# Kernel tuning notes

Measured on AMD Instinct MI355X. Metric: run time of the kernel, lower is better.

Reference implementation:

```python
import jax, jax.numpy as jnp
import numpy as np

SR = 8                      # search_range
MO = 2 * SR + 1             # max_offset = 17
NC = MO * MO                # 289 cost-volume channels


def _l2_normalize(x, eps=1e-12):
    # torch F.normalize(p=2, dim=1): x / max(||x||_2, eps)
    n = jnp.sqrt(jnp.sum(x * x, axis=1, keepdims=True))
    return x / jnp.maximum(n, eps)


def _conv2d(x, w, b, pad, groups=1):
    out = jax.lax.conv_general_dilated(
        x, w, window_strides=(1, 1), padding=[(pad, pad), (pad, pad)],
        feature_group_count=groups,
        dimension_numbers=('NCHW', 'OIHW', 'NCHW'))
    return out + b[None, :, None, None]


def _cost_volume(x1, x2, sr, norm_both=False):
    x1 = _l2_normalize(x1)
    if norm_both:
        x2 = _l2_normalize(x2)
    bs, c, h, w = x1.shape
    padded = jnp.pad(x2, ((0, 0), (0, 0), (sr, sr), (sr, sr)))
    mo = 2 * sr + 1
    # offsets in (j outer, i inner) order, matching the original double loop
    jj, ii = jnp.meshgrid(jnp.arange(mo), jnp.arange(mo), indexing='ij')
    offs = jnp.stack([jj.reshape(-1), ii.reshape(-1)], axis=-1)  # [mo^2, 2]

    def step(carry, off):
        sl = jax.lax.dynamic_slice(padded, (0, 0, off[0], off[1]), (bs, c, h, w))
        return carry, jnp.mean(x1 * sl, axis=1)  # [bs, h, w]

    _, cv = jax.lax.scan(step, None, offs)       # [mo^2, bs, h, w]
    cv = jnp.transpose(cv, (1, 0, 2, 3))          # [bs, mo^2, h, w]
    return jax.nn.leaky_relu(cv, 0.1)


def setup_inputs() -> dict:
    key = jax.random.key(0)
    ks = jax.random.split(key, 8)
    bs, c, h, w = 4, 256, 64, 64
    scale = 0.05
    return {
        'f1': jax.random.normal(ks[0], (bs, c, h, w), jnp.float32),
        'f2': jax.random.normal(ks[1], (bs, c, h, w), jnp.float32),
        'att_w': jax.random.normal(ks[2], (NC, 1, 7, 7), jnp.float32) * scale,
        'att_b': jax.random.normal(ks[3], (NC,), jnp.float32) * scale,
        'agg1_w': jax.random.normal(ks[4], (NC // 2, NC, 3, 3), jnp.float32) * scale,
        'agg1_b': jax.random.normal(ks[5], (NC // 2,), jnp.float32) * scale,
        'agg2_w': jax.random.normal(ks[6], (49, NC // 2, 3, 3), jnp.float32) * scale,
        'agg2_b': jax.random.normal(ks[7], (49,), jnp.float32) * scale,
    }


def reference(f1, f2, att_w, att_b, agg1_w, agg1_b, agg2_w, agg2_b):
    match_vol = _cost_volume(f1, f2, SR, norm_both=False)          # [bs,289,h,w]
    att = _conv2d(match_vol, att_w, att_b, pad=3, groups=NC)       # depthwise 7x7
    att_vol = match_vol * att
    h1 = jax.nn.relu(_conv2d(att_vol, agg1_w, agg1_b, pad=1))      # Conv(289->144,3)
    out = jax.nn.relu(_conv2d(h1, agg2_w, agg2_b, pad=1))          # Conv(144->49,3)
    return out
```

## Files before the change

kernel.cpp:

```cpp
#include <hip/hip_runtime.h>
#include <hip/hip_bf16.h>

#define BS   4
#define C    256
#define HW   4096
#define NPIX 16384
#define NCH  289
#define MO   17
#define PH   80
#define PW   80
#define C1   144
#define C2   49
#define ASTR 264
#define ICP  320
#define IC3  192
#define CVP  70
#define CVC  320
#define CH64 72

typedef __bf16  bf16x8 __attribute__((ext_vector_type(8)));
typedef float   f32x4  __attribute__((ext_vector_type(4)));
typedef unsigned short us8 __attribute__((ext_vector_type(8)));

__device__ __forceinline__ void halo_zero_dev(unsigned short* p, int H, int halo,
                                              int Cc, int blk, int t) {
    int W = H;
    int inter = H - 2 * halo;
    int total_pos = H * W - inter * inter;
    int chunks = Cc >> 3;
    size_t tot = (size_t)total_pos * chunks * BS;
    size_t idx = (size_t)blk * 256 + t;
    if (idx >= tot) return;
    int c8 = (int)(idx % chunks);
    size_t r = idx / chunks;
    int pos = (int)(r % total_pos);
    int b = (int)(r / total_pos);
    int h, w;
    int topbot = 2 * halo * W;
    if (pos < halo * W) { h = pos / W; w = pos % W; }
    else if (pos < topbot) { int q = pos - halo * W; h = H - halo + q / W; w = q % W; }
    else {
        int q = pos - topbot;
        int row = q / (2 * halo), off = q % (2 * halo);
        h = halo + row;
        w = (off < halo) ? off : (W - 2 * halo + off);
    }
    us8 z = {0, 0, 0, 0, 0, 0, 0, 0};
    *(us8*)&p[(((size_t)b * H + h) * W + w) * Cc + c8 * 8] = z;
}

__global__ void setup_kernel(unsigned short* __restrict__ x2bf, unsigned short* __restrict__ cvp,
                             unsigned short* __restrict__ avp, unsigned short* __restrict__ h1p,
                             const float* __restrict__ w1, unsigned short* __restrict__ wb1,
                             const float* __restrict__ w2, unsigned short* __restrict__ wb2,
                             const float* __restrict__ att_w, float* __restrict__ wdwp,
                             const float* __restrict__ f1, unsigned short* __restrict__ x1bf,
                             const float* __restrict__ f2) {
    __shared__ float shmem[16 * 257 + 16];
    int blk = blockIdx.x;
    int t = threadIdx.x;
    if (blk < 4030) {
        if (blk < 1152) { halo_zero_dev(x2bf, PH, 8, C, blk, t); return; }
        if (blk < 1655) { halo_zero_dev(cvp, CVP, 3, CVC, blk - 1152, t); return; }
        if (blk < 1818) { halo_zero_dev(avp, 66, 1, ICP, blk - 1655, t); return; }
        if (blk < 1916) { halo_zero_dev(h1p, 66, 1, IC3, blk - 1818, t); return; }
        if (blk < 3536) {
            int idx = (blk - 1916) * 256 + t;
            int tap = idx / (C1 * ICP);
            int r = idx - tap * (C1 * ICP);
            int oc = r / ICP;
            int ic = r - oc * ICP;
            float v = (ic < NCH) ? w1[((size_t)(oc * NCH + ic)) * 9 + tap] : 0.f;
            __hip_bfloat16 hb = __float2bfloat16(v);
            wb1[idx] = *(unsigned short*)&hb;
            return;
        }
        if (blk < 3968) {
            int idx = (blk - 3536) * 256 + t;
            int tap = idx / (64 * IC3);
            int r = idx - tap * (64 * IC3);
            int oc = r / IC3;
            int ic = r - oc * IC3;
            float v = (oc < C2 && ic < C1) ? w2[((size_t)(oc * C1 + ic)) * 9 + tap] : 0.f;
            __hip_bfloat16 hb = __float2bfloat16(v);
            wb2[idx] = *(unsigned short*)&hb;
            return;
        }
        {
            int idx = (blk - 3968) * 256 + t;
            if (idx >= 49 * CVC) return;
            int tap = idx / CVC;
            int ch = idx - tap * CVC;
            wdwp[idx] = (ch < NCH) ? att_w[ch * 49 + tap] : 0.f;
        }
        return;
    }
    if (blk < 5054) {
        float* tileT = shmem;
        float* invS = shmem + 16 * 257;
        int bb = blk - 4030;
        int pblk = bb & 255, b = bb >> 8;
        int p0 = pblk * 16;
        int tx = t & 15, ty = t >> 4;
        const float* s = f1 + (size_t)b * C * HW;
#pragma unroll
        for (int i2 = 0; i2 < 16; ++i2) {
            int c = ty + 16 * i2;
            tileT[tx * 257 + c] = s[(size_t)c * HW + p0 + tx];
        }
        __syncthreads();
        int px = t >> 4;
        int l = t & 15;
        float ssum = 0.f;
#pragma unroll
        for (int j2 = 0; j2 < 16; ++j2) {
            float v = tileT[px * 257 + l + 16 * j2];
            ssum += v * v;
        }
        ssum += __shfl_xor(ssum, 1);
        ssum += __shfl_xor(ssum, 2);
        ssum += __shfl_xor(ssum, 4);
        ssum += __shfl_xor(ssum, 8);
        if (l == 0) invS[px] = 1.0f / fmaxf(sqrtf(ssum), 1e-12f);
        __syncthreads();
#pragma unroll 4
        for (int p = 0; p < 16; ++p) {
            float v = tileT[p * 257 + t] * invS[p];
            __hip_bfloat16 hb = __float2bfloat16(v);
            x1bf[((size_t)b * HW + p0 + p) * C + t] = *(unsigned short*)&hb;
        }
        return;
    }
    {
        float* tile = shmem;
        int bb = blk - 5054;
        int pblk = bb & 127;
        int cblk = (bb >> 7) & 7;
        int b    = bb >> 10;
        int tx = t & 31, ty = t >> 5;
        int c0 = cblk * 32, p0 = pblk * 32;
        const float* s = f2 + (size_t)b * C * HW;
#pragma unroll
        for (int i = 0; i < 4; ++i) {
            int c = c0 + ty + 8 * i;
            tile[(ty + 8 * i) * 33 + tx] = s[(size_t)c * HW + p0 + tx];
        }
        __syncthreads();
#pragma unroll
        for (int i = 0; i < 4; ++i) {
            int p = p0 + ty + 8 * i;
            float v = tile[tx * 33 + ty + 8 * i];
            int c = c0 + tx;
            int h = p >> 6, w = p & 63;
            __hip_bfloat16 hb = __float2bfloat16(v);
            x2bf[(((size_t)b * PH + h + 8) * PW + (w + 8)) * C + c] = *(unsigned short*)&hb;
        }
    }
}

__global__ __launch_bounds__(512, 2)
void cv_mfma_kernel(const unsigned short* __restrict__ x1b,
                    const unsigned short* __restrict__ x2b,
                    unsigned short* __restrict__ cvp) {
    __shared__ __align__(16) unsigned short x2s[2][32 * ASTR];
    int i = blockIdx.x;
    int xcd = i & 7;
    int j = i >> 3;
    int hp = xcd * 2 + (j & 1);
    int jj = j >> 1;
    int wseg = jj & 3;
    int b = jj >> 2;
    int h0 = hp * 4;
    int w0 = wseg * 16;
    int t = threadIdx.x;
    int wave = t >> 6, lane = t & 63;
    int lrow = lane & 15, quad = lane >> 4;
    int row_w = wave >> 1, ct = wave & 1;
    int h = h0 + row_w;
    int col_l = ct * 16 + lrow;

    const unsigned short* x1p = x1b + ((size_t)b * HW + h * 64 + w0) * C;
    bf16x8 a[8];
#pragma unroll
    for (int kk = 0; kk < 8; ++kk)
        a[kk] = *(const bf16x8*)&x1p[(size_t)lrow * C + kk * 32 + quad * 8];

    const unsigned short* x2base = x2b + (size_t)b * PH * PW * C;

    {
        const unsigned short* rowp = x2base + ((size_t)h0 * PW + w0) * C;
#pragma unroll
        for (int s = 0; s < 2; ++s) {
            int v = t + s * 512;
            int col = v >> 5, ch8 = v & 31;
            *(us8*)&x2s[0][col * ASTR + ch8 * 8] = *(const us8*)&rowp[(size_t)col * C + ch8 * 8];
        }
    }
    __syncthreads();

    for (int rr = 0; rr < 20; ++rr) {
        us8 pr[2];
        bool dop = (rr + 1 < 20);
        if (dop) {
            const unsigned short* rowp = x2base + ((size_t)(h0 + rr + 1) * PW + w0) * C;
#pragma unroll
            for (int s = 0; s < 2; ++s) {
                int v = t + s * 512;
                int col = v >> 5, ch8 = v & 31;
                pr[s] = *(const us8*)&rowp[(size_t)col * C + ch8 * 8];
            }
        }

        int dj = rr - row_w;
        if ((unsigned)dj <= 16u) {
            const unsigned short* xs = x2s[rr & 1];
            f32x4 acc = {0.f, 0.f, 0.f, 0.f};
#pragma unroll
            for (int kk = 0; kk < 8; ++kk) {
                bf16x8 bb = *(const bf16x8*)&xs[col_l * ASTR + kk * 32 + quad * 8];
                acc = __builtin_amdgcn_mfma_f32_16x16x32_bf16(a[kk], bb, acc, 0, 0, 0);
            }
#pragma unroll
            for (int r = 0; r < 4; ++r) {
                int px_l = quad * 4 + r;
                int di = col_l - px_l;
                if ((unsigned)di <= 16u) {
                    float v = acc[r] * (1.0f / 256.0f);
                    v = (v > 0.f) ? v : 0.1f * v;
                    __hip_bfloat16 hb = __float2bfloat16(v);
                    cvp[(((size_t)b * CVP + h + 3) * CVP + (w0 + px_l + 3)) * CVC + dj * MO + di] =
                        *(unsigned short*)&hb;
                }
            }
        }

        if (dop) {
            unsigned short* dst = x2s[(rr + 1) & 1];
#pragma unroll
            for (int s = 0; s < 2; ++s) {
                int v = t + s * 512;
                int col = v >> 5, ch8 = v & 31;
                *(us8*)&dst[col * ASTR + ch8 * 8] = pr[s];
            }
            __syncthreads();
        }
    }
}

__global__ __launch_bounds__(256, 4)
void dw_att_tiled(const unsigned short* __restrict__ cvp,
                  const float* __restrict__ wdwp,
                  const float* __restrict__ att_b, unsigned short* __restrict__ av_pad) {
    __shared__ __align__(16) unsigned short actS[14 * 14 * 64];
    __shared__ float wdwS[49 * 64];
    int i = blockIdx.x;
    int ty = i & 7;
    int j = i >> 3;
    int cc = j % 5;
    int rest = j / 5;
    int tx = rest & 7, b = rest >> 3;
    int x0 = tx * 8, y0 = ty * 8;
    int c0 = cc * 64;
    int t = threadIdx.x;

    const unsigned short* cvb = cvp + (((size_t)b * CVP + y0) * CVP + x0) * CVC + c0;
    for (int v = t; v < 14 * 14 * 8; v += 256) {
        int rc = v >> 3, c8v = v & 7;
        int yy = rc / 14, xx = rc - yy * 14;
        *(us8*)&actS[rc * 64 + c8v * 8] =
            *(const us8*)&cvb[((size_t)yy * CVP + xx) * CVC + c8v * 8];
    }
    for (int v = t; v < 49 * 64; v += 256) {
        int tap = v >> 6, ch = v & 63;
        wdwS[v] = wdwp[tap * CVC + c0 + ch];
    }
    __syncthreads();

    int pr2 = t & 31;
    int rowg = t >> 5;
    int chl0 = 2 * pr2;
    int ch0 = c0 + chl0;
    float bv0 = (ch0 < NCH) ? att_b[ch0] : 0.f;
    float bv1 = (ch0 + 1 < NCH) ? att_b[ch0 + 1] : 0.f;
    float acc0[8], acc1[8];
#pragma unroll
    for (int px = 0; px < 8; ++px) { acc0[px] = bv0; acc1[px] = bv1; }

    for (int dy = 0; dy < 7; ++dy) {
        float w0[7], w1[7];
#pragma unroll
        for (int dx = 0; dx < 7; ++dx) {
            float2 wv = *(const float2*)&wdwS[(dy * 7 + dx) * 64 + chl0];
            w0[dx] = wv.x; w1[dx] = wv.y;
        }
        int row = rowg + dy;
        float r0[14], r1[14];
#pragma unroll
        for (int xx = 0; xx < 14; ++xx) {
            unsigned u = *(const unsigned*)&actS[(row * 14 + xx) * 64 + chl0];
            r0[xx] = __uint_as_float(u << 16);
            r1[xx] = __uint_as_float(u & 0xffff0000u);
        }
#pragma unroll
        for (int dx = 0; dx < 7; ++dx)
#pragma unroll
            for (int px = 0; px < 8; ++px) {
                acc0[px] += r0[px + dx] * w0[dx];
                acc1[px] += r1[px + dx] * w1[dx];
            }
    }

    if (ch0 < NCH) {
        bool pair = (ch0 + 1 < NCH);
#pragma unroll
        for (int px = 0; px < 8; ++px) {
            unsigned u = *(const unsigned*)&actS[((rowg + 3) * 14 + (px + 3)) * 64 + chl0];
            float c0v = __uint_as_float(u << 16);
            float c1v = __uint_as_float(u & 0xffff0000u);
            __hip_bfloat16 h0 = __float2bfloat16(c0v * acc0[px]);
            __hip_bfloat16 h1 = __float2bfloat16(c1v * acc1[px]);
            size_t o = (((size_t)b * 66 + y0 + rowg + 1) * 66 + (x0 + px + 1)) * ICP + ch0;
            if (pair) {
                unsigned ov = ((unsigned)*(unsigned short*)&h1 << 16) | (unsigned)*(unsigned short*)&h0;
                *(unsigned*)&av_pad[o] = ov;
            } else {
                av_pad[o] = *(unsigned short*)&h0;
            }
        }
    }
}

__device__ __forceinline__ const unsigned short* b1ptr(const unsigned short* wb1, int m) {
    int dy = m / 15, rm = m % 15, cc = rm / 3, dx = rm % 3;
    return wb1 + ((size_t)(dy * 3 + dx) * C1) * ICP + cc * 64;
}

#define A1_BLOAD(S0, S1, S2, P)                                                      \
    S0 = *(const us8*)&(P)[(size_t)(t >> 3) * ICP + (t & 7) * 8];                    \
    { int v_ = t + 512; S1 = *(const us8*)&(P)[(size_t)(v_ >> 3) * ICP + (v_ & 7) * 8]; } \
    if (t < 128) { int v_ = t + 1024; S2 = *(const us8*)&(P)[(size_t)(v_ >> 3) * ICP + (v_ & 7) * 8]; }

#define A1_BWRITE(S0, S1, S2, D)                                                     \
    *(us8*)&(D)[(t >> 3) * CH64 + (t & 7) * 8] = S0;                                 \
    { int v_ = t + 512; *(us8*)&(D)[(v_ >> 3) * CH64 + (v_ & 7) * 8] = S1; }         \
    if (t < 128) { int v_ = t + 1024; *(us8*)&(D)[(v_ >> 3) * CH64 + (v_ & 7) * 8] = S2; }

__global__ __launch_bounds__(512, 2)
void agg1_mfma_kernel(const unsigned short* __restrict__ av_pad,
                      const unsigned short* __restrict__ wb1,
                      const float* __restrict__ bias,
                      unsigned short* __restrict__ h1p) {
    __shared__ __align__(16) unsigned short aS2[2][66 * CH64];
    __shared__ __align__(16) unsigned short bS[2][C1 * CH64];
    int i = blockIdx.x;
    int xcd = i & 7;
    int j = i >> 3;
    int h = xcd * 8 + (j & 7);
    int b = j >> 3;
    int t = threadIdx.x;
    int wave = t >> 6, lane = t & 63;
    int lrow = lane & 15, quad = lane >> 4;
    int og = wave & 3, mg = wave >> 2;
    int ot0 = (og == 0) ? 0 : (og * 2 + 1);
    int nt  = (og == 0) ? 3 : 2;

    f32x4 acc[2][3];
#pragma unroll
    for (int m = 0; m < 2; ++m)
#pragma unroll
        for (int ii = 0; ii < 3; ++ii) acc[m][ii] = (f32x4){0.f, 0.f, 0.f, 0.f};

    const unsigned short* avb = av_pad + (((size_t)b * 66 + h) * 66) * ICP;

    us8 bE0, bE1, bE2, bO0, bO1, bO2;
    us8 a0, a1;

    {
        us8 p0, p1, p2, q0, q1;
        const unsigned short* w0p = b1ptr(wb1, 0);
        A1_BLOAD(p0, p1, p2, w0p)
        q0 = *(const us8*)&avb[(size_t)(t >> 3) * ICP + (t & 7) * 8];
        if (t < 16) { int v_ = t + 512; q1 = *(const us8*)&avb[(size_t)(v_ >> 3) * ICP + (v_ & 7) * 8]; }
        A1_BLOAD(bO0, bO1, bO2, b1ptr(wb1, 1))
        A1_BWRITE(p0, p1, p2, bS[0])
        *(us8*)&aS2[0][(t >> 3) * CH64 + (t & 7) * 8] = q0;
        if (t < 16) { int v_ = t + 512; *(us8*)&aS2[0][(v_ >> 3) * CH64 + (v_ & 7) * 8] = q1; }
    }
    __syncthreads();

    for (int k = 0; k < 45; ++k) {
        int dx = k % 3;
        if (k < 43) {
            const unsigned short* wt = b1ptr(wb1, k + 2);
            if ((k & 1) == 0) { A1_BLOAD(bE0, bE1, bE2, wt) }
            else              { A1_BLOAD(bO0, bO1, bO2, wt) }
        }
        if (dx == 0 && k < 42) {
            int p = k / 3 + 1;
            const unsigned short* ar = avb + (size_t)(p / 5) * 66 * ICP + (p % 5) * 64;
            a0 = *(const us8*)&ar[(size_t)(t >> 3) * ICP + (t & 7) * 8];
            if (t < 16) { int v_ = t + 512; a1 = *(const us8*)&ar[(size_t)(v_ >> 3) * ICP + (v_ & 7) * 8]; }
        }
        const unsigned short* aP = aS2[(k / 3) & 1];
        const unsigned short* bP = bS[k & 1];
#pragma unroll
        for (int c2 = 0; c2 < 2; ++c2) {
            bf16x8 bfr[3];
#pragma unroll
            for (int ii = 0; ii < 3; ++ii)
                if (ii < nt)
                    bfr[ii] = *(const bf16x8*)&bP[((ot0 + ii) * 16 + lrow) * CH64 + c2 * 32 + quad * 8];
#pragma unroll
            for (int m = 0; m < 2; ++m) {
                bf16x8 af = *(const bf16x8*)&aP[((mg * 2 + m) * 16 + lrow + dx) * CH64 + c2 * 32 + quad * 8];
#pragma unroll
                for (int ii = 0; ii < 3; ++ii)
                    if (ii < nt)
                        acc[m][ii] = __builtin_amdgcn_mfma_f32_16x16x32_bf16(af, bfr[ii], acc[m][ii], 0, 0, 0);
            }
        }
        if (k < 44) {
            unsigned short* dst = bS[(k + 1) & 1];
            if (((k + 1) & 1) == 0) { A1_BWRITE(bE0, bE1, bE2, dst) }
            else                    { A1_BWRITE(bO0, bO1, bO2, dst) }
            if (dx == 2) {
                unsigned short* adst = aS2[(k / 3 + 1) & 1];
                *(us8*)&adst[(t >> 3) * CH64 + (t & 7) * 8] = a0;
                if (t < 16) { int v_ = t + 512; *(us8*)&adst[(v_ >> 3) * CH64 + (v_ & 7) * 8] = a1; }
            }
            __syncthreads();
        }
    }

    size_t rowbase = ((size_t)b * 66 + h + 1) * 66;
#pragma unroll
    for (int m = 0; m < 2; ++m)
#pragma unroll
        for (int ii = 0; ii < 3; ++ii)
            if (ii < nt) {
                int oc = (ot0 + ii) * 16 + lrow;
                float bv = bias[oc];
#pragma unroll
                for (int r = 0; r < 4; ++r) {
                    int wl = (mg * 2 + m) * 16 + quad * 4 + r;
                    float val = fmaxf(acc[m][ii][r] + bv, 0.f);
                    __hip_bfloat16 hb = __float2bfloat16(val);
                    h1p[(rowbase + (wl + 1)) * IC3 + oc] = *(unsigned short*)&hb;
                }
            }
}

__device__ __forceinline__ const unsigned short* b2ptr(const unsigned short* wb2, int m) {
    int dy = m / 9, rm = m % 9, cc = rm / 3, dx = rm % 3;
    return wb2 + ((size_t)(dy * 3 + dx) * 64) * IC3 + cc * 64;
}

#define A2_BLOAD(S0, S1, P)                                                          \
    S0 = *(const us8*)&(P)[(size_t)(t >> 3) * IC3 + (t & 7) * 8];                    \
    { int v_ = t + 256; S1 = *(const us8*)&(P)[(size_t)(v_ >> 3) * IC3 + (v_ & 7) * 8]; }

#define A2_BWRITE(S0, S1, D)                                                         \
    *(us8*)&(D)[(t >> 3) * CH64 + (t & 7) * 8] = S0;                                 \
    { int v_ = t + 256; *(us8*)&(D)[(v_ >> 3) * CH64 + (v_ & 7) * 8] = S1; }

__global__ __launch_bounds__(256, 1)
void agg2_mfma_kernel(const unsigned short* __restrict__ h1p,
                      const unsigned short* __restrict__ wb2,
                      const float* __restrict__ bias, float* __restrict__ out) {
    __shared__ __align__(16) unsigned short aS2[2][66 * CH64];
    __shared__ __align__(16) unsigned short bS2[2][64 * CH64];
    int i = blockIdx.x;
    int xcd = i & 7;
    int j = i >> 3;
    int h = xcd * 8 + (j & 7);
    int b = j >> 3;
    int t = threadIdx.x;
    int wave = t >> 6, lane = t & 63;
    int lrow = lane & 15, quad = lane >> 4;
    int pt = wave;

    f32x4 acc[4];
#pragma unroll
    for (int ot = 0; ot < 4; ++ot) acc[ot] = (f32x4){0.f, 0.f, 0.f, 0.f};

    const unsigned short* h1b = h1p + (((size_t)b * 66 + h) * 66) * IC3;

    us8 bE0, bE1, bO0, bO1;
    us8 a0, a1, a2;

    {
        us8 p0, p1, q0, q1, q2;
        A2_BLOAD(p0, p1, wb2)
        q0 = *(const us8*)&h1b[(size_t)(t >> 3) * IC3 + (t & 7) * 8];
        { int v_ = t + 256; q1 = *(const us8*)&h1b[(size_t)(v_ >> 3) * IC3 + (v_ & 7) * 8]; }
        if (t < 16) { int v_ = t + 512; q2 = *(const us8*)&h1b[(size_t)(v_ >> 3) * IC3 + (v_ & 7) * 8]; }
        A2_BLOAD(bO0, bO1, b2ptr(wb2, 1))
        A2_BWRITE(p0, p1, bS2[0])
        *(us8*)&aS2[0][(t >> 3) * CH64 + (t & 7) * 8] = q0;
        { int v_ = t + 256; *(us8*)&aS2[0][(v_ >> 3) * CH64 + (v_ & 7) * 8] = q1; }
        if (t < 16) { int v_ = t + 512; *(us8*)&aS2[0][(v_ >> 3) * CH64 + (v_ & 7) * 8] = q2; }
    }
    __syncthreads();

    for (int k = 0; k < 27; ++k) {
        int dx = k % 3;
        if (k < 25) {
            const unsigned short* wt = b2ptr(wb2, k + 2);
            if ((k & 1) == 0) { A2_BLOAD(bE0, bE1, wt) }
            else              { A2_BLOAD(bO0, bO1, wt) }
        }
        if (dx == 0 && k < 24) {
            int p = k / 3 + 1;
            const unsigned short* ar = h1b + (size_t)(p / 3) * 66 * IC3 + (p % 3) * 64;
            a0 = *(const us8*)&ar[(size_t)(t >> 3) * IC3 + (t & 7) * 8];
            { int v_ = t + 256; a1 = *(const us8*)&ar[(size_t)(v_ >> 3) * IC3 + (v_ & 7) * 8]; }
            if (t < 16) { int v_ = t + 512; a2 = *(const us8*)&ar[(size_t)(v_ >> 3) * IC3 + (v_ & 7) * 8]; }
        }
        const unsigned short* aP = aS2[(k / 3) & 1];
        const unsigned short* bP = bS2[k & 1];
#pragma unroll
        for (int c2 = 0; c2 < 2; ++c2) {
            bf16x8 af = *(const bf16x8*)&aP[(pt * 16 + lrow + dx) * CH64 + c2 * 32 + quad * 8];
#pragma unroll
            for (int ot = 0; ot < 4; ++ot) {
                bf16x8 bfr = *(const bf16x8*)&bP[(ot * 16 + lrow) * CH64 + c2 * 32 + quad * 8];
                acc[ot] = __builtin_amdgcn_mfma_f32_16x16x32_bf16(af, bfr, acc[ot], 0, 0, 0);
            }
        }
        if (k < 26) {
            unsigned short* dst = bS2[(k + 1) & 1];
            if (((k + 1) & 1) == 0) { A2_BWRITE(bE0, bE1, dst) }
            else                    { A2_BWRITE(bO0, bO1, dst) }
            if (dx == 2) {
                unsigned short* adst = aS2[(k / 3 + 1) & 1];
                *(us8*)&adst[(t >> 3) * CH64 + (t & 7) * 8] = a0;
                { int v_ = t + 256; *(us8*)&adst[(v_ >> 3) * CH64 + (v_ & 7) * 8] = a1; }
                if (t < 16) { int v_ = t + 512; *(us8*)&adst[(v_ >> 3) * CH64 + (v_ & 7) * 8] = a2; }
            }
            __syncthreads();
        }
    }

#pragma unroll
    for (int ot = 0; ot < 4; ++ot) {
        int o = ot * 16 + lrow;
        if (o < C2) {
            float bv = bias[o];
#pragma unroll
            for (int r = 0; r < 4; ++r) {
                int w = pt * 16 + quad * 4 + r;
                out[((size_t)b * C2 + o) * HW + h * 64 + w] = fmaxf(acc[ot][r] + bv, 0.f);
            }
        }
    }
}

extern "C" void kernel_launch(void* const* d_in, const int* in_sizes, int n_in,
                              void* d_out, int out_size, void* d_ws, size_t ws_size,
                              hipStream_t stream) {
    const float* f1    = (const float*)d_in[0];
    const float* f2    = (const float*)d_in[1];
    const float* att_w = (const float*)d_in[2];
    const float* att_b = (const float*)d_in[3];
    const float* w1    = (const float*)d_in[4];
    const float* b1    = (const float*)d_in[5];
    const float* w2    = (const float*)d_in[6];
    const float* b2    = (const float*)d_in[7];
    float* out = (float*)d_out;

    char* wsb = (char*)d_ws;
    size_t off = 0;
    float* wdwp = (float*)(wsb + off); off += (size_t)49 * CVC * 4;
    off = (off + 15) & ~(size_t)15;
    unsigned short* x1bf = (unsigned short*)(wsb + off); off += (size_t)NPIX * C * 2;
    unsigned short* x2bf = (unsigned short*)(wsb + off); off += (size_t)BS * PH * PW * C * 2;
    unsigned short* cvp  = (unsigned short*)(wsb + off); off += (size_t)BS * CVP * CVP * CVC * 2;
    unsigned short* avp  = (unsigned short*)(wsb + off); off += (size_t)BS * 66 * 66 * ICP * 2;
    unsigned short* wb1  = (unsigned short*)(wsb + off); off += (size_t)9 * C1 * ICP * 2;
    unsigned short* h1p  = (unsigned short*)(wsb + off); off += (size_t)BS * 66 * 66 * IC3 * 2;
    unsigned short* wb2  = (unsigned short*)(wsb + off); off += (size_t)9 * 64 * IC3 * 2;
    if (ws_size < off) return;

    setup_kernel<<<9150, 256, 0, stream>>>(x2bf, cvp, avp, h1p, w1, wb1, w2, wb2,
                                           att_w, wdwp, f1, x1bf, f2);
    cv_mfma_kernel<<<256, 512, 0, stream>>>(x1bf, x2bf, cvp);
    dw_att_tiled<<<1280, 256, 0, stream>>>(cvp, wdwp, att_b, avp);
    agg1_mfma_kernel<<<256, 512, 0, stream>>>(avp, wb1, b1, h1p);
    agg2_mfma_kernel<<<256, 256, 0, stream>>>(h1p, wb2, b2, out);
}
```

Baseline: 190.0 us.

## Stage conv tiles via direct global-to-LDS loads with XOR-swizzled layout

Both aggregation conv kernels now fill shared memory with global_load_lds (direct global-to-LDS DMA) instead of loading into registers and writing back to LDS. The padded LDS row stride is replaced by a 64-wide layout with an XOR swizzle to avoid bank conflicts. Fragment reads are hoisted before the MFMA batch. The aim is to cut register pressure and VALU/LDS-store work, and to overlap copies with compute. The trade-off is a shorter prefetch distance: it drops from two stages to one, and the copy must complete before the barrier.

```diff
diff --git a/kernel.cpp b/kernel.cpp
--- a/kernel.cpp
+++ b/kernel.cpp
@@ -21,6 +21,12 @@
 typedef __bf16  bf16x8 __attribute__((ext_vector_type(8)));
 typedef float   f32x4  __attribute__((ext_vector_type(4)));
 typedef unsigned short us8 __attribute__((ext_vector_type(8)));
+
+__device__ __forceinline__ void gload16(const unsigned short* g, unsigned short* l) {
+    __builtin_amdgcn_global_load_lds(
+        (const __attribute__((address_space(1))) unsigned int*)g,
+        (__attribute__((address_space(3))) unsigned int*)l, 16, 0, 0);
+}
 
 __device__ __forceinline__ void halo_zero_dev(unsigned short* p, int H, int halo,
                                               int Cc, int blk, int t) {
@@ -335,23 +341,13 @@
     return wb1 + ((size_t)(dy * 3 + dx) * C1) * ICP + cc * 64;
 }
 
-#define A1_BLOAD(S0, S1, S2, P)                                                      \
-    S0 = *(const us8*)&(P)[(size_t)(t >> 3) * ICP + (t & 7) * 8];                    \
-    { int v_ = t + 512; S1 = *(const us8*)&(P)[(size_t)(v_ >> 3) * ICP + (v_ & 7) * 8]; } \
-    if (t < 128) { int v_ = t + 1024; S2 = *(const us8*)&(P)[(size_t)(v_ >> 3) * ICP + (v_ & 7) * 8]; }
-
-#define A1_BWRITE(S0, S1, S2, D)                                                     \
-    *(us8*)&(D)[(t >> 3) * CH64 + (t & 7) * 8] = S0;                                 \
-    { int v_ = t + 512; *(us8*)&(D)[(v_ >> 3) * CH64 + (v_ & 7) * 8] = S1; }         \
-    if (t < 128) { int v_ = t + 1024; *(us8*)&(D)[(v_ >> 3) * CH64 + (v_ & 7) * 8] = S2; }
-
 __global__ __launch_bounds__(512, 2)
 void agg1_mfma_kernel(const unsigned short* __restrict__ av_pad,
                       const unsigned short* __restrict__ wb1,
                       const float* __restrict__ bias,
                       unsigned short* __restrict__ h1p) {
-    __shared__ __align__(16) unsigned short aS2[2][66 * CH64];
-    __shared__ __align__(16) unsigned short bS[2][C1 * CH64];
+    __shared__ __align__(16) unsigned short aS[2][72 * 64];
+    __shared__ __align__(16) unsigned short bS[2][144 * 64];
     int i = blockIdx.x;
     int xcd = i & 7;
     int j = i >> 3;
@@ -363,6 +359,8 @@
     int og = wave & 3, mg = wave >> 2;
     int ot0 = (og == 0) ? 0 : (og * 2 + 1);
     int nt  = (og == 0) ? 3 : 2;
+    int g_row = lane >> 3;
+    int g_sl  = ((lane & 7) ^ g_row) << 3;
 
     f32x4 acc[2][3];
 #pragma unroll
@@ -372,64 +370,60 @@
 
     const unsigned short* avb = av_pad + (((size_t)b * 66 + h) * 66) * ICP;
 
-    us8 bE0, bE1, bE2, bO0, bO1, bO2;
-    us8 a0, a1;
-
     {
-        us8 p0, p1, p2, q0, q1;
-        const unsigned short* w0p = b1ptr(wb1, 0);
-        A1_BLOAD(p0, p1, p2, w0p)
-        q0 = *(const us8*)&avb[(size_t)(t >> 3) * ICP + (t & 7) * 8];
-        if (t < 16) { int v_ = t + 512; q1 = *(const us8*)&avb[(size_t)(v_ >> 3) * ICP + (v_ & 7) * 8]; }
-        A1_BLOAD(bO0, bO1, bO2, b1ptr(wb1, 1))
-        A1_BWRITE(p0, p1, p2, bS[0])
-        *(us8*)&aS2[0][(t >> 3) * CH64 + (t & 7) * 8] = q0;
-        if (t < 16) { int v_ = t + 512; *(us8*)&aS2[0][(v_ >> 3) * CH64 + (v_ & 7) * 8] = q1; }
+        const unsigned short* wt = b1ptr(wb1, 0);
+        for (int s = wave; s < 18; s += 8)
+            gload16(wt + (size_t)(s * 8 + g_row) * ICP + g_sl, &bS[0][s * 512]);
+        for (int s = wave; s < 9; s += 8)
+            gload16(avb + (size_t)(s * 8 + g_row) * ICP + g_sl, &aS[0][s * 512]);
     }
     __syncthreads();
 
     for (int k = 0; k < 45; ++k) {
         int dx = k % 3;
-        if (k < 43) {
-            const unsigned short* wt = b1ptr(wb1, k + 2);
-            if ((k & 1) == 0) { A1_BLOAD(bE0, bE1, bE2, wt) }
-            else              { A1_BLOAD(bO0, bO1, bO2, wt) }
+        if (k < 44) {
+            const unsigned short* wt = b1ptr(wb1, k + 1);
+            unsigned short* dst = &bS[(k + 1) & 1][0];
+            for (int s = wave; s < 18; s += 8)
+                gload16(wt + (size_t)(s * 8 + g_row) * ICP + g_sl, dst + s * 512);
         }
         if (dx == 0 && k < 42) {
             int p = k / 3 + 1;
             const unsigned short* ar = avb + (size_t)(p / 5) * 66 * ICP + (p % 5) * 64;
-            a0 = *(const us8*)&ar[(size_t)(t >> 3) * ICP + (t & 7) * 8];
-            if (t < 16) { int v_ = t + 512; a1 = *(const us8*)&ar[(size_t)(v_ >> 3) * ICP + (v_ & 7) * 8]; }
-        }
-        const unsigned short* aP = aS2[(k / 3) & 1];
+            unsigned short* dst = &aS[p & 1][0];
+            for (int s = wave; s < 9; s += 8)
+                gload16(ar + (size_t)(s * 8 + g_row) * ICP + g_sl, dst + s * 512);
+        }
+        const unsigned short* aP = aS[(k / 3) & 1];
         const unsigned short* bP = bS[k & 1];
+        int swa = (lrow + dx) & 7;
+        int swb = lrow & 7;
+        bf16x8 afr[2][2], bfr[3][2];
 #pragma unroll
         for (int c2 = 0; c2 < 2; ++c2) {
-            bf16x8 bfr[3];
+            int sl = c2 * 4 + quad;
+#pragma unroll
+            for (int m = 0; m < 2; ++m) {
+                int P = (mg * 2 + m) * 16 + lrow + dx;
+                afr[m][c2] = *(const bf16x8*)&aP[P * 64 + ((sl ^ swa) << 3)];
+            }
 #pragma unroll
             for (int ii = 0; ii < 3; ++ii)
-                if (ii < nt)
-                    bfr[ii] = *(const bf16x8*)&bP[((ot0 + ii) * 16 + lrow) * CH64 + c2 * 32 + quad * 8];
-#pragma unroll
-            for (int m = 0; m < 2; ++m) {
-                bf16x8 af = *(const bf16x8*)&aP[((mg * 2 + m) * 16 + lrow + dx) * CH64 + c2 * 32 + quad * 8];
+                if (ii < nt) {
+                    int R = (ot0 + ii) * 16 + lrow;
+                    bfr[ii][c2] = *(const bf16x8*)&bP[R * 64 + ((sl ^ swb) << 3)];
+                }
+        }
+#pragma unroll
+        for (int c2 = 0; c2 < 2; ++c2)
+#pragma unroll
+            for (int m = 0; m < 2; ++m)
 #pragma unroll
                 for (int ii = 0; ii < 3; ++ii)
                     if (ii < nt)
-                        acc[m][ii] = __builtin_amdgcn_mfma_f32_16x16x32_bf16(af, bfr[ii], acc[m][ii], 0, 0, 0);
-            }
-        }
-        if (k < 44) {
-            unsigned short* dst = bS[(k + 1) & 1];
-            if (((k + 1) & 1) == 0) { A1_BWRITE(bE0, bE1, bE2, dst) }
-            else                    { A1_BWRITE(bO0, bO1, bO2, dst) }
-            if (dx == 2) {
-                unsigned short* adst = aS2[(k / 3 + 1) & 1];
-                *(us8*)&adst[(t >> 3) * CH64 + (t & 7) * 8] = a0;
-                if (t < 16) { int v_ = t + 512; *(us8*)&adst[(v_ >> 3) * CH64 + (v_ & 7) * 8] = a1; }
-            }
-            __syncthreads();
-        }
+                        acc[m][ii] = __builtin_amdgcn_mfma_f32_16x16x32_bf16(
+                            afr[m][c2], bfr[ii][c2], acc[m][ii], 0, 0, 0);
+        if (k < 44) __syncthreads();
     }
 
     size_t rowbase = ((size_t)b * 66 + h + 1) * 66;
@@ -455,20 +449,12 @@
     return wb2 + ((size_t)(dy * 3 + dx) * 64) * IC3 + cc * 64;
 }
 
-#define A2_BLOAD(S0, S1, P)                                                          \
-    S0 = *(const us8*)&(P)[(size_t)(t >> 3) * IC3 + (t & 7) * 8];                    \
-    { int v_ = t + 256; S1 = *(const us8*)&(P)[(size_t)(v_ >> 3) * IC3 + (v_ & 7) * 8]; }
-
-#define A2_BWRITE(S0, S1, D)                                                         \
-    *(us8*)&(D)[(t >> 3) * CH64 + (t & 7) * 8] = S0;                                 \
-    { int v_ = t + 256; *(us8*)&(D)[(v_ >> 3) * CH64 + (v_ & 7) * 8] = S1; }
-
 __global__ __launch_bounds__(256, 1)
 void agg2_mfma_kernel(const unsigned short* __restrict__ h1p,
                       const unsigned short* __restrict__ wb2,
                       const float* __restrict__ bias, float* __restrict__ out) {
-    __shared__ __align__(16) unsigned short aS2[2][66 * CH64];
-    __shared__ __align__(16) unsigned short bS2[2][64 * CH64];
+    __shared__ __align__(16) unsigned short aS[2][72 * 64];
+    __shared__ __align__(16) unsigned short bS2[2][64 * 64];
     int i = blockIdx.x;
     int xcd = i & 7;
     int j = i >> 3;
@@ -478,6 +464,8 @@
     int wave = t >> 6, lane = t & 63;
     int lrow = lane & 15, quad = lane >> 4;
     int pt = wave;
+    int g_row = lane >> 3;
+    int g_sl  = ((lane & 7) ^ g_row) << 3;
 
     f32x4 acc[4];
 #pragma unroll
@@ -485,60 +473,54 @@
 
     const unsigned short* h1b = h1p + (((size_t)b * 66 + h) * 66) * IC3;
 
-    us8 bE0, bE1, bO0, bO1;
-    us8 a0, a1, a2;
-
     {
-        us8 p0, p1, q0, q1, q2;
-        A2_BLOAD(p0, p1, wb2)
-        q0 = *(const us8*)&h1b[(size_t)(t >> 3) * IC3 + (t & 7) * 8];
-        { int v_ = t + 256; q1 = *(const us8*)&h1b[(size_t)(v_ >> 3) * IC3 + (v_ & 7) * 8]; }
-        if (t < 16) { int v_ = t + 512; q2 = *(const us8*)&h1b[(size_t)(v_ >> 3) * IC3 + (v_ & 7) * 8]; }
-        A2_BLOAD(bO0, bO1, b2ptr(wb2, 1))
-        A2_BWRITE(p0, p1, bS2[0])
-        *(us8*)&aS2[0][(t >> 3) * CH64 + (t & 7) * 8] = q0;
-        { int v_ = t + 256; *(us8*)&aS2[0][(v_ >> 3) * CH64 + (v_ & 7) * 8] = q1; }
-        if (t < 16) { int v_ = t + 512; *(us8*)&aS2[0][(v_ >> 3) * CH64 + (v_ & 7) * 8] = q2; }
+        for (int s = wave; s < 8; s += 4)
+            gload16(wb2 + (size_t)(s * 8 + g_row) * IC3 + g_sl, &bS2[0][s * 512]);
+        for (int s = wave; s < 9; s += 4)
+            gload16(h1b + (size_t)(s * 8 + g_row) * IC3 + g_sl, &aS[0][s * 512]);
     }
     __syncthreads();
 
     for (int k = 0; k < 27; ++k) {
         int dx = k % 3;
-        if (k < 25) {
-            const unsigned short* wt = b2ptr(wb2, k + 2);
-            if ((k & 1) == 0) { A2_BLOAD(bE0, bE1, wt) }
-            else              { A2_BLOAD(bO0, bO1, wt) }
+        if (k < 26) {
+            const unsigned short* wt = b2ptr(wb2, k + 1);
+            unsigned short* dst = &bS2[(k + 1) & 1][0];
+            for (int s = wave; s < 8; s += 4)
+                gload16(wt + (size_t)(s * 8 + g_row) * IC3 + g_sl, dst + s * 512);
         }
         if (dx == 0 && k < 24) {
             int p = k / 3 + 1;
             const unsigned short* ar = h1b + (size_t)(p / 3) * 66 * IC3 + (p % 3) * 64;
-            a0 = *(const us8*)&ar[(size_t)(t >> 3) * IC3 + (t & 7) * 8];
-            { int v_ = t + 256; a1 = *(const us8*)&ar[(size_t)(v_ >> 3) * IC3 + (v_ & 7) * 8]; }
-            if (t < 16) { int v_ = t + 512; a2 = *(const us8*)&ar[(size_t)(v_ >> 3) * IC3 + (v_ & 7) * 8]; }
-        }
-        const unsigned short* aP = aS2[(k / 3) & 1];
+            unsigned short* dst = &aS[p & 1][0];
+            for (int s = wave; s < 9; s += 4)
+                gload16(ar + (size_t)(s * 8 + g_row) * IC3 + g_sl, dst + s * 512);
+        }
+        const unsigned short* aP = aS[(k / 3) & 1];
         const unsigned short* bP = bS2[k & 1];
+        int swa = (lrow + dx) & 7;
+        int swb = lrow & 7;
+        bf16x8 afr[2], bfr[4][2];
 #pragma unroll
         for (int c2 = 0; c2 < 2; ++c2) {
-            bf16x8 af = *(const bf16x8*)&aP[(pt * 16 + lrow + dx) * CH64 + c2 * 32 + quad * 8];
+            int sl = c2 * 4 + quad;
+            {
+                int P = pt * 16 + lrow + dx;
+                afr[c2] = *(const bf16x8*)&aP[P * 64 + ((sl ^ swa) << 3)];
+            }
 #pragma unroll
             for (int ot = 0; ot < 4; ++ot) {
-                bf16x8 bfr = *(const bf16x8*)&bP[(ot * 16 + lrow) * CH64 + c2 * 32 + quad * 8];
-                acc[ot] = __builtin_amdgcn_mfma_f32_16x16x32_bf16(af, bfr, acc[ot], 0, 0, 0);
-            }
-        }
-        if (k < 26) {
-            unsigned short* dst = bS2[(k + 1) & 1];
-            if (((k + 1) & 1) == 0) { A2_BWRITE(bE0, bE1, dst) }
-            else                    { A2_BWRITE(bO0, bO1, dst) }
-            if (dx == 2) {
-                unsigned short* adst = aS2[(k / 3 + 1) & 1];
-                *(us8*)&adst[(t >> 3) * CH64 + (t & 7) * 8] = a0;
-                { int v_ = t + 256; *(us8*)&adst[(v_ >> 3) * CH64 + (v_ & 7) * 8] = a1; }
-                if (t < 16) { int v_ = t + 512; *(us8*)&adst[(v_ >> 3) * CH64 + (v_ & 7) * 8] = a2; }
-            }
-            __syncthreads();
-        }
+                int R = ot * 16 + lrow;
+                bfr[ot][c2] = *(const bf16x8*)&bP[R * 64 + ((sl ^ swb) << 3)];
+            }
+        }
+#pragma unroll
+        for (int c2 = 0; c2 < 2; ++c2)
+#pragma unroll
+            for (int ot = 0; ot < 4; ++ot)
+                acc[ot] = __builtin_amdgcn_mfma_f32_16x16x32_bf16(
+                    afr[c2], bfr[ot][c2], acc[ot], 0, 0, 0);
+        if (k < 26) __syncthreads();
     }
 
 #pragma unroll
```

Result: no change. 191.6 us (+0.8%).
